# Kernel tuning notes

Measured on AMD Instinct MI355X. Metric: run time of the kernel, lower is better.

Reference implementation:

```python
import jax, jax.numpy as jnp
import numpy as np

# MACE TensorProductConv with in_irreps=128x0e, sh_irreps=0e+1o+2e+3o,
# every CG path 0e (x) l -> l is the identity, so the fused tensor product is
# out[e, c, (l, m)] = w[e, l, c] * x_src[e, c] * sh[e, (l, m)].
# SymmetricContraction is a stub (pass) in the given source, treated as identity.

N_SRC = 10000
N_DST = 10000
E = 100000
C = 128           # channel multiplicity
LS = (0, 1, 2, 3) # spherical-harmonic degrees; dims 1,3,5,7 -> sh dim 16
SH_DIM = sum(2 * l + 1 for l in LS)
MLP_IN = 64
MLP_HID = 128
W_NUMEL = len(LS) * C  # 512 tensor-product weights per edge


def setup_inputs() -> dict:
    key = jax.random.key(0)
    ks = jax.random.split(key, 7)
    return {
        "src_features": jax.random.normal(ks[0], (N_SRC, C), dtype=jnp.float32),
        "edge_sh": jax.random.normal(ks[1], (E, SH_DIM), dtype=jnp.float32),
        "edge_emb": jax.random.normal(ks[2], (E, MLP_IN), dtype=jnp.float32),
        "W1": jax.random.normal(ks[3], (MLP_IN, MLP_HID), dtype=jnp.float32),
        "W2": jax.random.normal(ks[4], (MLP_HID, W_NUMEL), dtype=jnp.float32),
        "src": jax.random.randint(ks[5], (E,), 0, N_SRC),
        "dst": jax.random.randint(ks[6], (E,), 0, N_DST),
        "num_dst_nodes": N_DST,
    }


def _mlp(edge_emb, W1, W2):
    # e3nn FullyConnectedNet: normalized linear layers, silu on hidden only.
    h = jax.nn.silu(edge_emb @ (W1 / np.sqrt(MLP_IN)))
    return h @ (W2 / np.sqrt(MLP_HID))  # [E, W_NUMEL]


def reference(src_features, edge_sh, edge_emb, W1, W2, src, dst, num_dst_nodes):
    tp_w = _mlp(edge_emb, W1, W2).reshape(-1, len(LS), C)  # [E, L, C]
    x_src = src_features[src]                                # gather: [E, C]
    outs = []
    off = 0
    for i, l in enumerate(LS):
        d = 2 * l + 1
        sh_l = edge_sh[:, off:off + d]                       # [E, d]
        # weighted scalar-times-SH tensor product: [E, C, d]
        o = (tp_w[:, i, :] * x_src)[:, :, None] * sh_l[:, None, :]
        outs.append(o.reshape(o.shape[0], C * d))
        off += d
    out_e = jnp.concatenate(outs, axis=-1)                   # [E, 2048]
    # scatter-reduce sum onto destination nodes
    node_out = jax.ops.segment_sum(out_e, dst, num_segments=num_dst_nodes)
    # SymmetricContraction stub -> identity
    return node_out
```

## Files before the change

### kernel.cpp

```cpp
#include <hip/hip_runtime.h>
#include <math.h>

#define C_DIM 128
#define SHD   16
#define HID   128
#define MIN_D 64
#define OUT_PER_NODE 2048
#define BLK   256
#define MBLK  512
#define SCAN_T 1024
#define MT    128

#define HST 136

typedef __attribute__((ext_vector_type(8))) short bf16x8;
typedef __attribute__((ext_vector_type(4))) float f32x4;

__device__ __forceinline__ unsigned f2bf_u(float x) {
    unsigned u = __builtin_bit_cast(unsigned, x);
    return (u + 0x7fffu + ((u >> 16) & 1u)) >> 16;
}
__device__ __forceinline__ short f2bf(float x) { return (short)f2bf_u(x); }
__device__ __forceinline__ unsigned packbf2(float a, float b) {
    return f2bf_u(a) | (f2bf_u(b) << 16);
}
__device__ __forceinline__ float bf2f(unsigned h) {
    return __builtin_bit_cast(float, h << 16);
}

__global__ void prep_kernel(const int* __restrict__ dst, int* counts, int E,
                            const float* __restrict__ W1, const float* __restrict__ W2,
                            short* __restrict__ w1t, short* __restrict__ w2t,
                            int HB) {
    int b = blockIdx.x;
    int t = threadIdx.x;
    if (b < HB) {
        int i = b * BLK + t;
        if (i < E) atomicAdd(&counts[dst[i]], 1);
    } else {
        int i = (b - HB) * BLK + t;
        if (i < MIN_D * HID) {
            int n = i >> 6, k = i & 63;
            w1t[i] = f2bf(W1[k * HID + n] * 0.125f);
        } else if (i < MIN_D * HID + HID * 512) {
            int j = i - MIN_D * HID;
            int p = j >> 7, ks = j & 127;
            int nt = p >> 4, m16 = p & 15;
            int jcol = 32 * (nt >> 1) + 2 * m16 + (nt & 1);
            int ka   = (2 * (ks >> 5) + (ks & 1)) * 16 + ((ks >> 1) & 15);
            w2t[j] = f2bf(W2[ka * 512 + jcol] * 0.0883883476483184f);
        }
    }
}

__global__ __launch_bounds__(SCAN_T)
void scan_kernel(const int* __restrict__ counts, int* row_ptr, int* cursor, int n) {
    const int t = threadIdx.x;
    const int per = (n + SCAN_T - 1) / SCAN_T;
    int lp[16];
    int base = t * per;
    int sum = 0;
    for (int i = 0; i < per && i < 16; ++i) {
        int idx = base + i;
        int v = (idx < n) ? counts[idx] : 0;
        lp[i] = sum;
        sum += v;
    }
    __shared__ int sbuf[SCAN_T];
    sbuf[t] = sum;
    __syncthreads();
    for (int off = 1; off < SCAN_T; off <<= 1) {
        int v = (t >= off) ? sbuf[t - off] : 0;
        __syncthreads();
        sbuf[t] += v;
        __syncthreads();
    }
    int excl = (t == 0) ? 0 : sbuf[t - 1];
    for (int i = 0; i < per && i < 16; ++i) {
        int idx = base + i;
        if (idx < n) {
            int rp = excl + lp[i];
            row_ptr[idx] = rp;
            cursor[idx]  = rp;
        }
    }
    if (t == SCAN_T - 1) row_ptr[n] = sbuf[SCAN_T - 1];
}

__global__ void scatter_kernel(const int* __restrict__ dst, const int* __restrict__ src,
                               int* cursor, int2* es_list, int E) {
    int i = blockIdx.x * blockDim.x + threadIdx.x;
    if (i < E) {
        int pos = atomicAdd(&cursor[dst[i]], 1);
        es_list[pos] = make_int2(i, src[i]);
    }
}

__global__ __launch_bounds__(MBLK)
void mlp_kernel(const float* __restrict__ edge_emb,
                const short* __restrict__ w1t,
                const short* __restrict__ w2t,
                unsigned* __restrict__ tp_u,
                int E)
{
    const int t    = threadIdx.x;
    const int lane = t & 63;
    const int w    = t >> 6;
    const int m16  = lane & 15;
    const int q    = lane >> 4;
    const int e0   = blockIdx.x * MT;

    __shared__ __align__(16) short hb[MT * HST];
    unsigned* hb_u = (unsigned*)hb;

    union CVT { unsigned u[4]; bf16x8 v; };

    bf16x8 a[2];
    {
        const int row = e0 + w * 16 + m16;
        if (row < E) {
            const float* rp = &edge_emb[(size_t)row * MIN_D];
#pragma unroll
            for (int ks = 0; ks < 2; ++ks) {
                float4 v0 = *(const float4*)&rp[ks * 32 + q * 8];
                float4 v1 = *(const float4*)&rp[ks * 32 + q * 8 + 4];
                CVT c;
                c.u[0] = packbf2(v0.x, v0.y);
                c.u[1] = packbf2(v0.z, v0.w);
                c.u[2] = packbf2(v1.x, v1.y);
                c.u[3] = packbf2(v1.z, v1.w);
                a[ks] = c.v;
            }
        } else {
            CVT c; c.u[0] = c.u[1] = c.u[2] = c.u[3] = 0u;
            a[0] = c.v; a[1] = c.v;
        }
    }

#pragma unroll
    for (int u2 = 0; u2 < 4; ++u2) {
        f32x4 c0 = {0.f, 0.f, 0.f, 0.f}, c1 = {0.f, 0.f, 0.f, 0.f};
#pragma unroll
        for (int ks = 0; ks < 2; ++ks) {
            bf16x8 b0 = *(const bf16x8*)&w1t[((2 * u2) * 16 + m16) * MIN_D + ks * 32 + q * 8];
            bf16x8 b1 = *(const bf16x8*)&w1t[((2 * u2 + 1) * 16 + m16) * MIN_D + ks * 32 + q * 8];
            c0 = __builtin_amdgcn_mfma_f32_16x16x32_bf16(a[ks], b0, c0, 0, 0, 0);
            c1 = __builtin_amdgcn_mfma_f32_16x16x32_bf16(a[ks], b1, c1, 0, 0, 0);
        }
#pragma unroll
        for (int r = 0; r < 4; ++r) {
            int hrow = w * 16 + q * 4 + r;
            float z0 = c0[r], z1 = c1[r];
            float h0 = z0 / (1.f + __expf(-z0));
            float h1 = z1 / (1.f + __expf(-z1));
            hb_u[hrow * (HST / 2) + 16 * u2 + m16] = packbf2(h0, h1);
        }
    }

    bf16x8 B[4][4];
#pragma unroll
    for (int j = 0; j < 4; ++j)
#pragma unroll
        for (int ks = 0; ks < 4; ++ks)
            B[j][ks] = *(const bf16x8*)&w2t[((4 * w + j) * 16 + m16) * HID + ks * 32 + q * 8];

    __syncthreads();

    for (int mt = 0; mt < 8; ++mt) {
        bf16x8 av[4];
#pragma unroll
        for (int ks = 0; ks < 4; ++ks)
            av[ks] = *(const bf16x8*)&hb[(mt * 16 + m16) * HST + ks * 32 + q * 8];
        f32x4 acc[4];
#pragma unroll
        for (int j = 0; j < 4; ++j) acc[j] = (f32x4){0.f, 0.f, 0.f, 0.f};
#pragma unroll
        for (int ks = 0; ks < 4; ++ks)
#pragma unroll
            for (int j = 0; j < 4; ++j)
                acc[j] = __builtin_amdgcn_mfma_f32_16x16x32_bf16(av[ks], B[j][ks], acc[j], 0, 0, 0);
#pragma unroll
        for (int i = 0; i < 2; ++i) {
            const int p = 2 * w + i;
#pragma unroll
            for (int r = 0; r < 4; ++r) {
                int e = e0 + mt * 16 + q * 4 + r;
                if (e < E)
                    tp_u[(size_t)e * 256 + 16 * p + m16] = packbf2(acc[2 * i][r], acc[2 * i + 1][r]);
            }
        }
    }
}

template<int L>
__device__ __forceinline__ void tp_node(
    const float* __restrict__ src_features,
    const float* __restrict__ edge_sh,
    const unsigned* __restrict__ tp_u,
    const int2* __restrict__ es_list,
    float* __restrict__ out,
    int n, int t, int rbeg, int rend)
{
    constexpr int D = 2 * L + 1;
    constexpr int SHOFF = L * L;
    const int c0 = (2 * t) & 127;
    const int obase = 128 * L * L + c0 * D;

    float accA[D], accB[D];
#pragma unroll
    for (int m = 0; m < D; ++m) { accA[m] = 0.f; accB[m] = 0.f; }

    int i = rbeg;
    for (; i + 4 <= rend; i += 4) {
        int2 es[4];
#pragma unroll
        for (int k = 0; k < 4; ++k) es[k] = es_list[i + k];
        unsigned tp2[4]; float2 x[4]; float sh[4][D];
#pragma unroll
        for (int k = 0; k < 4; ++k) {
            tp2[k] = tp_u[(size_t)es[k].x * 256 + t];
            x[k]   = *(const float2*)&src_features[(size_t)es[k].y * C_DIM + c0];
            const float* shp = &edge_sh[(size_t)es[k].x * SHD + SHOFF];
#pragma unroll
            for (int m = 0; m < D; ++m) sh[k][m] = shp[m];
        }
#pragma unroll
        for (int k = 0; k < 4; ++k) {
            float wx0 = bf2f(tp2[k] & 0xffffu) * x[k].x;
            float wx1 = bf2f(tp2[k] >> 16)     * x[k].y;
#pragma unroll
            for (int m = 0; m < D; ++m) {
                accA[m] += wx0 * sh[k][m];
                accB[m] += wx1 * sh[k][m];
            }
        }
    }
    for (; i < rend; ++i) {
        int2 es = es_list[i];
        unsigned tp2 = tp_u[(size_t)es.x * 256 + t];
        float2 x = *(const float2*)&src_features[(size_t)es.y * C_DIM + c0];
        float wx0 = bf2f(tp2 & 0xffffu) * x.x;
        float wx1 = bf2f(tp2 >> 16)     * x.y;
        const float* shp = &edge_sh[(size_t)es.x * SHD + SHOFF];
#pragma unroll
        for (int m = 0; m < D; ++m) {
            float sh = shp[m];
            accA[m] += wx0 * sh;
            accB[m] += wx1 * sh;
        }
    }

    float* op = out + (size_t)n * OUT_PER_NODE + obase;
#pragma unroll
    for (int m = 0; m < D; ++m) op[m] = accA[m];
#pragma unroll
    for (int m = 0; m < D; ++m) op[D + m] = accB[m];
}

__global__ __launch_bounds__(BLK)
void tp_kernel(const float* __restrict__ src_features,
               const float* __restrict__ edge_sh,
               const unsigned* __restrict__ tp_u,
               const int* __restrict__ row_ptr,
               const int2* __restrict__ es_list,
               float* __restrict__ out)
{
    const int n = blockIdx.x;
    const int t = threadIdx.x;
    const int l = t >> 6;
    const int rbeg = row_ptr[n];
    const int rend = row_ptr[n + 1];
    if (l == 0)      tp_node<0>(src_features, edge_sh, tp_u, es_list, out, n, t, rbeg, rend);
    else if (l == 1) tp_node<1>(src_features, edge_sh, tp_u, es_list, out, n, t, rbeg, rend);
    else if (l == 2) tp_node<2>(src_features, edge_sh, tp_u, es_list, out, n, t, rbeg, rend);
    else             tp_node<3>(src_features, edge_sh, tp_u, es_list, out, n, t, rbeg, rend);
}


extern "C" void kernel_launch(void* const* d_in, const int* in_sizes, int n_in,
                              void* d_out, int out_size, void* d_ws, size_t ws_size,
                              hipStream_t stream) {
    const float* src_features = (const float*)d_in[0];
    const float* edge_sh      = (const float*)d_in[1];
    const float* edge_emb     = (const float*)d_in[2];
    const float* W1           = (const float*)d_in[3];
    const float* W2           = (const float*)d_in[4];
    const int*   src          = (const int*)d_in[5];
    const int*   dst          = (const int*)d_in[6];

    const int E     = in_sizes[5];
    const int N_DST = out_size / OUT_PER_NODE;
    const int EB    = (E + MT - 1) / MT;

    char* p = (char*)d_ws;
    short* w1t      = (short*)p;              p += MIN_D * HID * 2;
    short* w2t      = (short*)p;              p += HID * 512 * 2;
    unsigned* tp_u  = (unsigned*)p;           p += (size_t)EB * MT * 1024;
    int2* es_list   = (int2*)p;               p += (size_t)E * 8;
    int* counts     = (int*)p;                p += 16384 * 4;
    int* row_ptr    = (int*)p;                p += 16384 * 4;
    int* cursor     = (int*)p;                p += 16384 * 4;

    const int HB = (E + BLK - 1) / BLK;
    const int CB = (MIN_D * HID + HID * 512 + BLK - 1) / BLK;

    (void)hipMemsetAsync(counts, 0, (size_t)N_DST * 4, stream);
    prep_kernel<<<HB + CB, BLK, 0, stream>>>(dst, counts, E, W1, W2, w1t, w2t, HB);
    scan_kernel<<<1, SCAN_T, 0, stream>>>(counts, row_ptr, cursor, N_DST);
    scatter_kernel<<<(E + 255) / 256, 256, 0, stream>>>(dst, src, cursor, es_list, E);
    mlp_kernel<<<EB, MBLK, 0, stream>>>(edge_emb, w1t, w2t, tp_u, E);
    tp_kernel<<<N_DST, BLK, 0, stream>>>(src_features, edge_sh, tp_u,
                                         row_ptr, es_list, (float*)d_out);
}
```

Baseline: 231.7 us.

## Fuse edge MLP with tensor-product scatter over dst-sorted edge blocks

Merges the MLP and the tensor-product/aggregation kernels into one kernel. Each block handles 64 consecutive dst-sorted edges, computes their MLP weights into LDS, and reduces them per destination segment, so the per-edge bf16 weight buffer no longer makes a round trip through global memory. A new seg_zero kernel builds per-block segment lists and zero-fills nodes whose edges span several blocks. Those split nodes are accumulated with float atomics, which adds atomic traffic and makes summation order non-deterministic. LDS use per block rises to roughly 80KB, which may limit occupancy.

```diff
diff --git a/kernel.cpp b/kernel.cpp
--- a/kernel.cpp
+++ b/kernel.cpp
@@ -7,11 +7,8 @@
 #define MIN_D 64
 #define OUT_PER_NODE 2048
 #define BLK   256
-#define MBLK  512
 #define SCAN_T 1024
-#define MT    128
-
-#define HST 136
+#define EBLK  64
 
 typedef __attribute__((ext_vector_type(8))) short bf16x8;
 typedef __attribute__((ext_vector_type(4))) float f32x4;
@@ -46,7 +43,7 @@
             int j = i - MIN_D * HID;
             int p = j >> 7, ks = j & 127;
             int nt = p >> 4, m16 = p & 15;
-            int jcol = 32 * (nt >> 1) + 2 * m16 + (nt & 1);
+            int jcol = 64 * (nt >> 2) + 4 * m16 + (nt & 3);
             int ka   = (2 * (ks >> 5) + (ks & 1)) * 16 + ((ks >> 1) & 15);
             w2t[j] = f2bf(W2[ka * 512 + jcol] * 0.0883883476483184f);
         }
@@ -96,30 +93,142 @@
     }
 }
 
-__global__ __launch_bounds__(MBLK)
-void mlp_kernel(const float* __restrict__ edge_emb,
-                const short* __restrict__ w1t,
-                const short* __restrict__ w2t,
-                unsigned* __restrict__ tp_u,
-                int E)
+__global__ __launch_bounds__(BLK)
+void seg_zero_kernel(const int* __restrict__ row_ptr, unsigned* __restrict__ seg,
+                     int* __restrict__ segcnt, float* __restrict__ out, int n_dst) {
+    const int n = blockIdx.x;
+    const int t = threadIdx.x;
+    const int rb = row_ptr[n], re = row_ptr[n + 1];
+    if (rb == re) {
+        float4 z = make_float4(0.f, 0.f, 0.f, 0.f);
+        float4* op = (float4*)(out + (size_t)n * OUT_PER_NODE);
+        for (int i = t; i < OUT_PER_NODE / 4; i += BLK) op[i] = z;
+        return;
+    }
+    const int b0 = rb >> 6, b1 = (re - 1) >> 6;
+    const bool full = (b0 == b1);
+    if (t == 0) {
+        for (int b = b0; b <= b1; ++b) {
+            int s = rb - b * EBLK; if (s < 0) s = 0;
+            int e = re - b * EBLK; if (e > EBLK) e = EBLK;
+            int idx = atomicAdd(&segcnt[b], 1);
+            if (idx < EBLK)
+                seg[(size_t)b * EBLK + idx] =
+                    (unsigned)n | ((unsigned)s << 16) | ((unsigned)e << 22)
+                                | (full ? (1u << 31) : 0u);
+        }
+    }
+    if (!full) {
+        float4 z = make_float4(0.f, 0.f, 0.f, 0.f);
+        float4* op = (float4*)(out + (size_t)n * OUT_PER_NODE);
+        for (int i = t; i < OUT_PER_NODE / 4; i += BLK) op[i] = z;
+    }
+}
+
+template<int L>
+__device__ __forceinline__ void tp_seg(
+    const float* __restrict__ src_features,
+    const float* __restrict__ edge_sh,
+    const unsigned* tp_lds,
+    const int2* __restrict__ es_list,
+    float* __restrict__ out,
+    int n, int tq, int p0, int s, int e, bool full)
+{
+    constexpr int D = 2 * L + 1;
+    constexpr int SHOFF = L * L;
+    const int c0 = (2 * tq) & 127;
+
+    float accA[D], accB[D];
+#pragma unroll
+    for (int m = 0; m < D; ++m) { accA[m] = 0.f; accB[m] = 0.f; }
+
+    int i = s;
+    for (; i + 4 <= e; i += 4) {
+        int2 es[4];
+#pragma unroll
+        for (int k = 0; k < 4; ++k) es[k] = es_list[p0 + i + k];
+        unsigned tp2[4]; float2 x[4]; float sh[4][D];
+#pragma unroll
+        for (int k = 0; k < 4; ++k) {
+            tp2[k] = tp_lds[(i + k) * 256 + tq];
+            x[k]   = *(const float2*)&src_features[(size_t)es[k].y * C_DIM + c0];
+            const float* shp = &edge_sh[(size_t)es[k].x * SHD + SHOFF];
+#pragma unroll
+            for (int m = 0; m < D; ++m) sh[k][m] = shp[m];
+        }
+#pragma unroll
+        for (int k = 0; k < 4; ++k) {
+            float wx0 = bf2f(tp2[k] & 0xffffu) * x[k].x;
+            float wx1 = bf2f(tp2[k] >> 16)     * x[k].y;
+#pragma unroll
+            for (int m = 0; m < D; ++m) {
+                accA[m] += wx0 * sh[k][m];
+                accB[m] += wx1 * sh[k][m];
+            }
+        }
+    }
+    for (; i < e; ++i) {
+        int2 es = es_list[p0 + i];
+        unsigned tp2 = tp_lds[i * 256 + tq];
+        float2 x = *(const float2*)&src_features[(size_t)es.y * C_DIM + c0];
+        const float* shp = &edge_sh[(size_t)es.x * SHD + SHOFF];
+        float wx0 = bf2f(tp2 & 0xffffu) * x.x;
+        float wx1 = bf2f(tp2 >> 16)     * x.y;
+#pragma unroll
+        for (int m = 0; m < D; ++m) {
+            float shv = shp[m];
+            accA[m] += wx0 * shv;
+            accB[m] += wx1 * shv;
+        }
+    }
+
+    float* op = out + (size_t)n * OUT_PER_NODE + 128 * SHOFF + c0 * D;
+    if (full) {
+#pragma unroll
+        for (int m = 0; m < D; ++m) op[m] = accA[m];
+#pragma unroll
+        for (int m = 0; m < D; ++m) op[D + m] = accB[m];
+    } else {
+#pragma unroll
+        for (int m = 0; m < D; ++m) atomicAdd(&op[m], accA[m]);
+#pragma unroll
+        for (int m = 0; m < D; ++m) atomicAdd(&op[D + m], accB[m]);
+    }
+}
+
+__global__ __launch_bounds__(512, 4)
+void fused_kernel(const float* __restrict__ edge_emb,
+                  const short* __restrict__ w1t,
+                  const short* __restrict__ w2t,
+                  const float* __restrict__ src_features,
+                  const float* __restrict__ edge_sh,
+                  const int2* __restrict__ es_list,
+                  const unsigned* __restrict__ seg,
+                  const int* __restrict__ segcnt,
+                  float* __restrict__ out,
+                  int E)
 {
     const int t    = threadIdx.x;
     const int lane = t & 63;
     const int w    = t >> 6;
     const int m16  = lane & 15;
     const int q    = lane >> 4;
-    const int e0   = blockIdx.x * MT;
-
-    __shared__ __align__(16) short hb[MT * HST];
-    unsigned* hb_u = (unsigned*)hb;
+    const int b    = blockIdx.x;
+    const int p0   = b * EBLK;
+
+    __shared__ __align__(16) unsigned tp_lds[EBLK * 256];
+    __shared__ __align__(16) unsigned hb[EBLK * 64];
 
     union CVT { unsigned u[4]; bf16x8 v; };
 
-    bf16x8 a[2];
     {
-        const int row = e0 + w * 16 + m16;
-        if (row < E) {
-            const float* rp = &edge_emb[(size_t)row * MIN_D];
+        const int mt = w & 3;
+        const int uh = w >> 2;
+        const int prow = p0 + mt * 16 + m16;
+        bf16x8 a[2];
+        if (prow < E) {
+            const int eid = es_list[prow].x;
+            const float* rp = &edge_emb[(size_t)eid * MIN_D];
 #pragma unroll
             for (int ks = 0; ks < 2; ++ks) {
                 float4 v0 = *(const float4*)&rp[ks * 32 + q * 8];
@@ -135,25 +244,25 @@
             CVT c; c.u[0] = c.u[1] = c.u[2] = c.u[3] = 0u;
             a[0] = c.v; a[1] = c.v;
         }
-    }
-
-#pragma unroll
-    for (int u2 = 0; u2 < 4; ++u2) {
-        f32x4 c0 = {0.f, 0.f, 0.f, 0.f}, c1 = {0.f, 0.f, 0.f, 0.f};
-#pragma unroll
-        for (int ks = 0; ks < 2; ++ks) {
-            bf16x8 b0 = *(const bf16x8*)&w1t[((2 * u2) * 16 + m16) * MIN_D + ks * 32 + q * 8];
-            bf16x8 b1 = *(const bf16x8*)&w1t[((2 * u2 + 1) * 16 + m16) * MIN_D + ks * 32 + q * 8];
-            c0 = __builtin_amdgcn_mfma_f32_16x16x32_bf16(a[ks], b0, c0, 0, 0, 0);
-            c1 = __builtin_amdgcn_mfma_f32_16x16x32_bf16(a[ks], b1, c1, 0, 0, 0);
-        }
-#pragma unroll
-        for (int r = 0; r < 4; ++r) {
-            int hrow = w * 16 + q * 4 + r;
-            float z0 = c0[r], z1 = c1[r];
-            float h0 = z0 / (1.f + __expf(-z0));
-            float h1 = z1 / (1.f + __expf(-z1));
-            hb_u[hrow * (HST / 2) + 16 * u2 + m16] = packbf2(h0, h1);
+#pragma unroll
+        for (int ui = 0; ui < 2; ++ui) {
+            const int u2 = 2 * uh + ui;
+            f32x4 c0 = {0.f, 0.f, 0.f, 0.f}, c1 = {0.f, 0.f, 0.f, 0.f};
+#pragma unroll
+            for (int ks = 0; ks < 2; ++ks) {
+                bf16x8 b0 = *(const bf16x8*)&w1t[((2 * u2)     * 16 + m16) * MIN_D + ks * 32 + q * 8];
+                bf16x8 b1 = *(const bf16x8*)&w1t[((2 * u2 + 1) * 16 + m16) * MIN_D + ks * 32 + q * 8];
+                c0 = __builtin_amdgcn_mfma_f32_16x16x32_bf16(a[ks], b0, c0, 0, 0, 0);
+                c1 = __builtin_amdgcn_mfma_f32_16x16x32_bf16(a[ks], b1, c1, 0, 0, 0);
+            }
+#pragma unroll
+            for (int r = 0; r < 4; ++r) {
+                const int row = mt * 16 + q * 4 + r;
+                float z0 = c0[r], z1 = c1[r];
+                float h0 = z0 / (1.f + __expf(-z0));
+                float h1 = z1 / (1.f + __expf(-z1));
+                hb[(row * 64 + 16 * u2 + m16) ^ ((row & 7) << 2)] = packbf2(h0, h1);
+            }
         }
     }
 
@@ -166,116 +275,54 @@
 
     __syncthreads();
 
-    for (int mt = 0; mt < 8; ++mt) {
-        bf16x8 av[4];
-#pragma unroll
-        for (int ks = 0; ks < 4; ++ks)
-            av[ks] = *(const bf16x8*)&hb[(mt * 16 + m16) * HST + ks * 32 + q * 8];
-        f32x4 acc[4];
-#pragma unroll
-        for (int j = 0; j < 4; ++j) acc[j] = (f32x4){0.f, 0.f, 0.f, 0.f};
-#pragma unroll
-        for (int ks = 0; ks < 4; ++ks)
-#pragma unroll
-            for (int j = 0; j < 4; ++j)
-                acc[j] = __builtin_amdgcn_mfma_f32_16x16x32_bf16(av[ks], B[j][ks], acc[j], 0, 0, 0);
-#pragma unroll
-        for (int i = 0; i < 2; ++i) {
-            const int p = 2 * w + i;
+    {
+        const int d0 = 64 * (w >> 1) + 32 * (w & 1) + 2 * m16;
+#pragma unroll
+        for (int mt = 0; mt < 4; ++mt) {
+            const int row = mt * 16 + m16;
+            bf16x8 av[4];
+#pragma unroll
+            for (int ks = 0; ks < 4; ++ks)
+                av[ks] = *(const bf16x8*)&hb[(row * 64 + ks * 16 + q * 4) ^ ((row & 7) << 2)];
+            f32x4 acc[4];
+#pragma unroll
+            for (int j = 0; j < 4; ++j) acc[j] = (f32x4){0.f, 0.f, 0.f, 0.f};
+#pragma unroll
+            for (int ks = 0; ks < 4; ++ks)
+#pragma unroll
+                for (int j = 0; j < 4; ++j)
+                    acc[j] = __builtin_amdgcn_mfma_f32_16x16x32_bf16(av[ks], B[j][ks], acc[j], 0, 0, 0);
 #pragma unroll
             for (int r = 0; r < 4; ++r) {
-                int e = e0 + mt * 16 + q * 4 + r;
-                if (e < E)
-                    tp_u[(size_t)e * 256 + 16 * p + m16] = packbf2(acc[2 * i][r], acc[2 * i + 1][r]);
-            }
-        }
-    }
-}
-
-template<int L>
-__device__ __forceinline__ void tp_node(
-    const float* __restrict__ src_features,
-    const float* __restrict__ edge_sh,
-    const unsigned* __restrict__ tp_u,
-    const int2* __restrict__ es_list,
-    float* __restrict__ out,
-    int n, int t, int rbeg, int rend)
-{
-    constexpr int D = 2 * L + 1;
-    constexpr int SHOFF = L * L;
-    const int c0 = (2 * t) & 127;
-    const int obase = 128 * L * L + c0 * D;
-
-    float accA[D], accB[D];
-#pragma unroll
-    for (int m = 0; m < D; ++m) { accA[m] = 0.f; accB[m] = 0.f; }
-
-    int i = rbeg;
-    for (; i + 4 <= rend; i += 4) {
-        int2 es[4];
-#pragma unroll
-        for (int k = 0; k < 4; ++k) es[k] = es_list[i + k];
-        unsigned tp2[4]; float2 x[4]; float sh[4][D];
-#pragma unroll
-        for (int k = 0; k < 4; ++k) {
-            tp2[k] = tp_u[(size_t)es[k].x * 256 + t];
-            x[k]   = *(const float2*)&src_features[(size_t)es[k].y * C_DIM + c0];
-            const float* shp = &edge_sh[(size_t)es[k].x * SHD + SHOFF];
-#pragma unroll
-            for (int m = 0; m < D; ++m) sh[k][m] = shp[m];
-        }
-#pragma unroll
-        for (int k = 0; k < 4; ++k) {
-            float wx0 = bf2f(tp2[k] & 0xffffu) * x[k].x;
-            float wx1 = bf2f(tp2[k] >> 16)     * x[k].y;
-#pragma unroll
-            for (int m = 0; m < D; ++m) {
-                accA[m] += wx0 * sh[k][m];
-                accB[m] += wx1 * sh[k][m];
-            }
-        }
-    }
-    for (; i < rend; ++i) {
-        int2 es = es_list[i];
-        unsigned tp2 = tp_u[(size_t)es.x * 256 + t];
-        float2 x = *(const float2*)&src_features[(size_t)es.y * C_DIM + c0];
-        float wx0 = bf2f(tp2 & 0xffffu) * x.x;
-        float wx1 = bf2f(tp2 >> 16)     * x.y;
-        const float* shp = &edge_sh[(size_t)es.x * SHD + SHOFF];
-#pragma unroll
-        for (int m = 0; m < D; ++m) {
-            float sh = shp[m];
-            accA[m] += wx0 * sh;
-            accB[m] += wx1 * sh;
-        }
-    }
-
-    float* op = out + (size_t)n * OUT_PER_NODE + obase;
-#pragma unroll
-    for (int m = 0; m < D; ++m) op[m] = accA[m];
-#pragma unroll
-    for (int m = 0; m < D; ++m) op[D + m] = accB[m];
-}
-
-__global__ __launch_bounds__(BLK)
-void tp_kernel(const float* __restrict__ src_features,
-               const float* __restrict__ edge_sh,
-               const unsigned* __restrict__ tp_u,
-               const int* __restrict__ row_ptr,
-               const int2* __restrict__ es_list,
-               float* __restrict__ out)
-{
-    const int n = blockIdx.x;
-    const int t = threadIdx.x;
-    const int l = t >> 6;
-    const int rbeg = row_ptr[n];
-    const int rend = row_ptr[n + 1];
-    if (l == 0)      tp_node<0>(src_features, edge_sh, tp_u, es_list, out, n, t, rbeg, rend);
-    else if (l == 1) tp_node<1>(src_features, edge_sh, tp_u, es_list, out, n, t, rbeg, rend);
-    else if (l == 2) tp_node<2>(src_features, edge_sh, tp_u, es_list, out, n, t, rbeg, rend);
-    else             tp_node<3>(src_features, edge_sh, tp_u, es_list, out, n, t, rbeg, rend);
-}
-
+                const int el = mt * 16 + q * 4 + r;
+                uint2 u;
+                u.x = packbf2(acc[0][r], acc[1][r]);
+                u.y = packbf2(acc[2][r], acc[3][r]);
+                *(uint2*)&tp_lds[el * 256 + d0] = u;
+            }
+        }
+    }
+
+    __syncthreads();
+
+    {
+        const int half = w >> 2;
+        const int tq   = t & 255;
+        const int l    = tq >> 6;
+        const int nseg = segcnt[b];
+        for (int k = half; k < nseg; k += 2) {
+            const unsigned sw = seg[(size_t)b * EBLK + k];
+            const int  n    = (int)(sw & 0xffffu);
+            const int  s    = (int)((sw >> 16) & 63u);
+            const int  e    = (int)((sw >> 22) & 127u);
+            const bool full = (sw >> 31) != 0u;
+            if (l == 0)      tp_seg<0>(src_features, edge_sh, tp_lds, es_list, out, n, tq, p0, s, e, full);
+            else if (l == 1) tp_seg<1>(src_features, edge_sh, tp_lds, es_list, out, n, tq, p0, s, e, full);
+            else if (l == 2) tp_seg<2>(src_features, edge_sh, tp_lds, es_list, out, n, tq, p0, s, e, full);
+            else             tp_seg<3>(src_features, edge_sh, tp_lds, es_list, out, n, tq, p0, s, e, full);
+        }
+    }
+}
 
 extern "C" void kernel_launch(void* const* d_in, const int* in_sizes, int n_in,
                               void* d_out, int out_size, void* d_ws, size_t ws_size,
@@ -290,25 +337,27 @@
 
     const int E     = in_sizes[5];
     const int N_DST = out_size / OUT_PER_NODE;
-    const int EB    = (E + MT - 1) / MT;
+    const int NB    = (E + EBLK - 1) / EBLK;
 
     char* p = (char*)d_ws;
-    short* w1t      = (short*)p;              p += MIN_D * HID * 2;
-    short* w2t      = (short*)p;              p += HID * 512 * 2;
-    unsigned* tp_u  = (unsigned*)p;           p += (size_t)EB * MT * 1024;
-    int2* es_list   = (int2*)p;               p += (size_t)E * 8;
-    int* counts     = (int*)p;                p += 16384 * 4;
-    int* row_ptr    = (int*)p;                p += 16384 * 4;
-    int* cursor     = (int*)p;                p += 16384 * 4;
+    short* w1t     = (short*)p;    p += MIN_D * HID * 2;
+    short* w2t     = (short*)p;    p += HID * 512 * 2;
+    int2* es_list  = (int2*)p;     p += (size_t)E * 8;
+    unsigned* seg  = (unsigned*)p; p += (size_t)NB * EBLK * 4;
+    int* counts    = (int*)p;      p += 16384 * 4;
+    int* row_ptr   = (int*)p;      p += 16384 * 4;
+    int* cursor    = (int*)p;      p += 16384 * 4;
+    int* segcnt    = (int*)p;      p += (size_t)NB * 4;
 
     const int HB = (E + BLK - 1) / BLK;
     const int CB = (MIN_D * HID + HID * 512 + BLK - 1) / BLK;
 
     (void)hipMemsetAsync(counts, 0, (size_t)N_DST * 4, stream);
+    (void)hipMemsetAsync(segcnt, 0, (size_t)NB * 4, stream);
     prep_kernel<<<HB + CB, BLK, 0, stream>>>(dst, counts, E, W1, W2, w1t, w2t, HB);
     scan_kernel<<<1, SCAN_T, 0, stream>>>(counts, row_ptr, cursor, N_DST);
     scatter_kernel<<<(E + 255) / 256, 256, 0, stream>>>(dst, src, cursor, es_list, E);
-    mlp_kernel<<<EB, MBLK, 0, stream>>>(edge_emb, w1t, w2t, tp_u, E);
-    tp_kernel<<<N_DST, BLK, 0, stream>>>(src_features, edge_sh, tp_u,
-                                         row_ptr, es_list, (float*)d_out);
-}
+    seg_zero_kernel<<<N_DST, BLK, 0, stream>>>(row_ptr, seg, segcnt, (float*)d_out, N_DST);
+    fused_kernel<<<NB, 512, 0, stream>>>(edge_emb, w1t, w2t, src_features, edge_sh,
+                                         es_list, seg, segcnt, (float*)d_out, E);
+}
```

Result: slower. 384.2 us (+65.8%).

## Fuse edge MLP into destination-grouped tensor-product kernel via LDS chunks

Applied to the files above, without the earlier changes.

Removes the separate MLP kernel and its per-edge bf16 weight buffer in global memory. The MLP now runs inside the convolution kernel on 16-edge chunks taken in CSR order, and the per-edge weights stay in LDS. Each block handles 4 destination nodes and walks their edges together, flushing accumulators at node boundaries. This avoids a large global write and re-read of tp weights, at the cost of redundant W2 register loads per chunk, extra barriers, and smaller MFMA batches.

```diff
diff --git a/kernel.cpp b/kernel.cpp
--- a/kernel.cpp
+++ b/kernel.cpp
@@ -7,11 +7,8 @@
 #define MIN_D 64
 #define OUT_PER_NODE 2048
 #define BLK   256
-#define MBLK  512
 #define SCAN_T 1024
-#define MT    128
-
-#define HST 136
+#define G     4
 
 typedef __attribute__((ext_vector_type(8))) short bf16x8;
 typedef __attribute__((ext_vector_type(4))) float f32x4;
@@ -46,7 +43,7 @@
             int j = i - MIN_D * HID;
             int p = j >> 7, ks = j & 127;
             int nt = p >> 4, m16 = p & 15;
-            int jcol = 32 * (nt >> 1) + 2 * m16 + (nt & 1);
+            int jcol = 128 * (nt >> 3) + 8 * m16 + (nt & 7);
             int ka   = (2 * (ks >> 5) + (ks & 1)) * 16 + ((ks >> 1) & 15);
             w2t[j] = f2bf(W2[ka * 512 + jcol] * 0.0883883476483184f);
         }
@@ -96,186 +93,218 @@
     }
 }
 
-__global__ __launch_bounds__(MBLK)
-void mlp_kernel(const float* __restrict__ edge_emb,
-                const short* __restrict__ w1t,
-                const short* __restrict__ w2t,
-                unsigned* __restrict__ tp_u,
-                int E)
+template<int L>
+__device__ __forceinline__ void tp_chunk(
+    const float* __restrict__ src_features,
+    const float* __restrict__ edge_sh,
+    const unsigned* tp_lds,
+    const int2* __restrict__ es_list,
+    const int* __restrict__ row_ptr,
+    float* __restrict__ out,
+    float* accA, float* accB, int& g, int& nextb,
+    int p0, int cnt, int n0, int n_valid, int tq)
+{
+    constexpr int D = 2 * L + 1;
+    constexpr int SHOFF = L * L;
+    const int c0 = (2 * tq) & 127;
+    int i = p0;
+    const int pend = p0 + cnt;
+    while (i < pend && g < n_valid) {
+        const int e = (nextb < pend) ? nextb : pend;
+        int il = i - p0;
+        while (i + 4 <= e) {
+            int2 es[4];
+#pragma unroll
+            for (int k = 0; k < 4; ++k) es[k] = es_list[i + k];
+            unsigned tp2[4]; float2 x[4]; float sh[4][D];
+#pragma unroll
+            for (int k = 0; k < 4; ++k) {
+                tp2[k] = tp_lds[(il + k) * 256 + tq];
+                x[k]   = *(const float2*)&src_features[(size_t)es[k].y * C_DIM + c0];
+                const float* shp = &edge_sh[(size_t)es[k].x * SHD + SHOFF];
+#pragma unroll
+                for (int m = 0; m < D; ++m) sh[k][m] = shp[m];
+            }
+#pragma unroll
+            for (int k = 0; k < 4; ++k) {
+                float wx0 = bf2f(tp2[k] & 0xffffu) * x[k].x;
+                float wx1 = bf2f(tp2[k] >> 16)     * x[k].y;
+#pragma unroll
+                for (int m = 0; m < D; ++m) {
+                    accA[m] += wx0 * sh[k][m];
+                    accB[m] += wx1 * sh[k][m];
+                }
+            }
+            i += 4; il += 4;
+        }
+        while (i < e) {
+            int2 es = es_list[i];
+            unsigned tp2 = tp_lds[il * 256 + tq];
+            float2 x = *(const float2*)&src_features[(size_t)es.y * C_DIM + c0];
+            const float* shp = &edge_sh[(size_t)es.x * SHD + SHOFF];
+            float wx0 = bf2f(tp2 & 0xffffu) * x.x;
+            float wx1 = bf2f(tp2 >> 16)     * x.y;
+#pragma unroll
+            for (int m = 0; m < D; ++m) {
+                float shv = shp[m];
+                accA[m] += wx0 * shv;
+                accB[m] += wx1 * shv;
+            }
+            ++i; ++il;
+        }
+        if (i == nextb) {
+            float* op = out + (size_t)(n0 + g) * OUT_PER_NODE + 128 * SHOFF + c0 * D;
+#pragma unroll
+            for (int m = 0; m < D; ++m) op[m] = accA[m];
+#pragma unroll
+            for (int m = 0; m < D; ++m) op[D + m] = accB[m];
+#pragma unroll
+            for (int m = 0; m < D; ++m) { accA[m] = 0.f; accB[m] = 0.f; }
+            ++g;
+            nextb = (g < n_valid) ? row_ptr[n0 + g + 1] : 0x7fffffff;
+        }
+    }
+}
+
+template<int L>
+__device__ __forceinline__ void tp_flush(
+    float* __restrict__ out, float* accA, float* accB,
+    int& g, int n_valid, int n0, int tq)
+{
+    constexpr int D = 2 * L + 1;
+    constexpr int SHOFF = L * L;
+    const int c0 = (2 * tq) & 127;
+    while (g < n_valid) {
+        float* op = out + (size_t)(n0 + g) * OUT_PER_NODE + 128 * SHOFF + c0 * D;
+#pragma unroll
+        for (int m = 0; m < D; ++m) op[m] = accA[m];
+#pragma unroll
+        for (int m = 0; m < D; ++m) op[D + m] = accB[m];
+#pragma unroll
+        for (int m = 0; m < D; ++m) { accA[m] = 0.f; accB[m] = 0.f; }
+        ++g;
+    }
+}
+
+__global__ __launch_bounds__(BLK, 4)
+void conv_kernel(const float* __restrict__ edge_emb,
+                 const short* __restrict__ w1t,
+                 const short* __restrict__ w2t,
+                 const float* __restrict__ src_features,
+                 const float* __restrict__ edge_sh,
+                 const int* __restrict__ row_ptr,
+                 const int2* __restrict__ es_list,
+                 float* __restrict__ out,
+                 int n_dst)
 {
     const int t    = threadIdx.x;
     const int lane = t & 63;
-    const int w    = t >> 6;
+    const int wv   = t >> 6;
     const int m16  = lane & 15;
     const int q    = lane >> 4;
-    const int e0   = blockIdx.x * MT;
-
-    __shared__ __align__(16) short hb[MT * HST];
-    unsigned* hb_u = (unsigned*)hb;
+
+    const int n0      = blockIdx.x * G;
+    const int n_valid = (n_dst - n0 < G) ? (n_dst - n0) : G;
+    const int rbeg    = row_ptr[n0];
+    const int rend    = row_ptr[n0 + n_valid];
+    const int nch     = (rend - rbeg + 15) >> 4;
+
+    __shared__ __align__(16) unsigned tp_lds[16 * 256];
+    __shared__ __align__(16) unsigned hb[1024];
 
     union CVT { unsigned u[4]; bf16x8 v; };
 
-    bf16x8 a[2];
-    {
-        const int row = e0 + w * 16 + m16;
-        if (row < E) {
-            const float* rp = &edge_emb[(size_t)row * MIN_D];
+    bf16x8 b1a[2], b1b[2];
+#pragma unroll
+    for (int ks = 0; ks < 2; ++ks) {
+        b1a[ks] = *(const bf16x8*)&w1t[((2 * wv)     * 16 + m16) * MIN_D + ks * 32 + q * 8];
+        b1b[ks] = *(const bf16x8*)&w1t[((2 * wv + 1) * 16 + m16) * MIN_D + ks * 32 + q * 8];
+    }
+
+    float accA[7], accB[7];
+#pragma unroll
+    for (int m = 0; m < 7; ++m) { accA[m] = 0.f; accB[m] = 0.f; }
+    int g     = 0;
+    int nextb = row_ptr[n0 + 1];
+
+    for (int c = 0; c < nch; ++c) {
+        const int p0  = rbeg + (c << 4);
+        const int cnt = (rend - p0 < 16) ? (rend - p0) : 16;
+
+        bf16x8 a[2];
+        if (m16 < cnt) {
+            const int eid = es_list[p0 + m16].x;
+            const float* rp = &edge_emb[(size_t)eid * MIN_D];
 #pragma unroll
             for (int ks = 0; ks < 2; ++ks) {
                 float4 v0 = *(const float4*)&rp[ks * 32 + q * 8];
                 float4 v1 = *(const float4*)&rp[ks * 32 + q * 8 + 4];
-                CVT c;
-                c.u[0] = packbf2(v0.x, v0.y);
-                c.u[1] = packbf2(v0.z, v0.w);
-                c.u[2] = packbf2(v1.x, v1.y);
-                c.u[3] = packbf2(v1.z, v1.w);
-                a[ks] = c.v;
+                CVT cc;
+                cc.u[0] = packbf2(v0.x, v0.y);
+                cc.u[1] = packbf2(v0.z, v0.w);
+                cc.u[2] = packbf2(v1.x, v1.y);
+                cc.u[3] = packbf2(v1.z, v1.w);
+                a[ks] = cc.v;
             }
         } else {
-            CVT c; c.u[0] = c.u[1] = c.u[2] = c.u[3] = 0u;
-            a[0] = c.v; a[1] = c.v;
-        }
-    }
-
-#pragma unroll
-    for (int u2 = 0; u2 < 4; ++u2) {
-        f32x4 c0 = {0.f, 0.f, 0.f, 0.f}, c1 = {0.f, 0.f, 0.f, 0.f};
+            CVT cc; cc.u[0] = cc.u[1] = cc.u[2] = cc.u[3] = 0u;
+            a[0] = cc.v; a[1] = cc.v;
+        }
+        f32x4 h0 = {0.f, 0.f, 0.f, 0.f}, h1 = {0.f, 0.f, 0.f, 0.f};
 #pragma unroll
         for (int ks = 0; ks < 2; ++ks) {
-            bf16x8 b0 = *(const bf16x8*)&w1t[((2 * u2) * 16 + m16) * MIN_D + ks * 32 + q * 8];
-            bf16x8 b1 = *(const bf16x8*)&w1t[((2 * u2 + 1) * 16 + m16) * MIN_D + ks * 32 + q * 8];
-            c0 = __builtin_amdgcn_mfma_f32_16x16x32_bf16(a[ks], b0, c0, 0, 0, 0);
-            c1 = __builtin_amdgcn_mfma_f32_16x16x32_bf16(a[ks], b1, c1, 0, 0, 0);
+            h0 = __builtin_amdgcn_mfma_f32_16x16x32_bf16(a[ks], b1a[ks], h0, 0, 0, 0);
+            h1 = __builtin_amdgcn_mfma_f32_16x16x32_bf16(a[ks], b1b[ks], h1, 0, 0, 0);
         }
 #pragma unroll
         for (int r = 0; r < 4; ++r) {
-            int hrow = w * 16 + q * 4 + r;
-            float z0 = c0[r], z1 = c1[r];
-            float h0 = z0 / (1.f + __expf(-z0));
-            float h1 = z1 / (1.f + __expf(-z1));
-            hb_u[hrow * (HST / 2) + 16 * u2 + m16] = packbf2(h0, h1);
-        }
-    }
-
-    bf16x8 B[4][4];
-#pragma unroll
-    for (int j = 0; j < 4; ++j)
-#pragma unroll
-        for (int ks = 0; ks < 4; ++ks)
-            B[j][ks] = *(const bf16x8*)&w2t[((4 * w + j) * 16 + m16) * HID + ks * 32 + q * 8];
-
-    __syncthreads();
-
-    for (int mt = 0; mt < 8; ++mt) {
-        bf16x8 av[4];
-#pragma unroll
-        for (int ks = 0; ks < 4; ++ks)
-            av[ks] = *(const bf16x8*)&hb[(mt * 16 + m16) * HST + ks * 32 + q * 8];
-        f32x4 acc[4];
-#pragma unroll
-        for (int j = 0; j < 4; ++j) acc[j] = (f32x4){0.f, 0.f, 0.f, 0.f};
-#pragma unroll
-        for (int ks = 0; ks < 4; ++ks)
-#pragma unroll
-            for (int j = 0; j < 4; ++j)
-                acc[j] = __builtin_amdgcn_mfma_f32_16x16x32_bf16(av[ks], B[j][ks], acc[j], 0, 0, 0);
-#pragma unroll
-        for (int i = 0; i < 2; ++i) {
-            const int p = 2 * w + i;
+            const int row = q * 4 + r;
+            float z0 = h0[r], z1 = h1[r];
+            float s0 = z0 / (1.f + __expf(-z0));
+            float s1 = z1 / (1.f + __expf(-z1));
+            hb[(row * 64 + 16 * wv + m16) ^ ((row & 7) << 2)] = packbf2(s0, s1);
+        }
+        __syncthreads();
+
+        {
+            bf16x8 av[4];
+#pragma unroll
+            for (int ks = 0; ks < 4; ++ks)
+                av[ks] = *(const bf16x8*)&hb[(m16 * 64 + ks * 16 + q * 4) ^ ((m16 & 7) << 2)];
+            f32x4 p[8];
+#pragma unroll
+            for (int j = 0; j < 8; ++j) p[j] = (f32x4){0.f, 0.f, 0.f, 0.f};
+#pragma unroll
+            for (int ks = 0; ks < 4; ++ks)
+#pragma unroll
+                for (int j = 0; j < 8; ++j) {
+                    bf16x8 B = *(const bf16x8*)&w2t[((8 * wv + j) * 16 + m16) * HID + ks * 32 + q * 8];
+                    p[j] = __builtin_amdgcn_mfma_f32_16x16x32_bf16(av[ks], B, p[j], 0, 0, 0);
+                }
 #pragma unroll
             for (int r = 0; r < 4; ++r) {
-                int e = e0 + mt * 16 + q * 4 + r;
-                if (e < E)
-                    tp_u[(size_t)e * 256 + 16 * p + m16] = packbf2(acc[2 * i][r], acc[2 * i + 1][r]);
-            }
-        }
-    }
-}
-
-template<int L>
-__device__ __forceinline__ void tp_node(
-    const float* __restrict__ src_features,
-    const float* __restrict__ edge_sh,
-    const unsigned* __restrict__ tp_u,
-    const int2* __restrict__ es_list,
-    float* __restrict__ out,
-    int n, int t, int rbeg, int rend)
-{
-    constexpr int D = 2 * L + 1;
-    constexpr int SHOFF = L * L;
-    const int c0 = (2 * t) & 127;
-    const int obase = 128 * L * L + c0 * D;
-
-    float accA[D], accB[D];
-#pragma unroll
-    for (int m = 0; m < D; ++m) { accA[m] = 0.f; accB[m] = 0.f; }
-
-    int i = rbeg;
-    for (; i + 4 <= rend; i += 4) {
-        int2 es[4];
-#pragma unroll
-        for (int k = 0; k < 4; ++k) es[k] = es_list[i + k];
-        unsigned tp2[4]; float2 x[4]; float sh[4][D];
-#pragma unroll
-        for (int k = 0; k < 4; ++k) {
-            tp2[k] = tp_u[(size_t)es[k].x * 256 + t];
-            x[k]   = *(const float2*)&src_features[(size_t)es[k].y * C_DIM + c0];
-            const float* shp = &edge_sh[(size_t)es[k].x * SHD + SHOFF];
-#pragma unroll
-            for (int m = 0; m < D; ++m) sh[k][m] = shp[m];
-        }
-#pragma unroll
-        for (int k = 0; k < 4; ++k) {
-            float wx0 = bf2f(tp2[k] & 0xffffu) * x[k].x;
-            float wx1 = bf2f(tp2[k] >> 16)     * x[k].y;
-#pragma unroll
-            for (int m = 0; m < D; ++m) {
-                accA[m] += wx0 * sh[k][m];
-                accB[m] += wx1 * sh[k][m];
-            }
-        }
-    }
-    for (; i < rend; ++i) {
-        int2 es = es_list[i];
-        unsigned tp2 = tp_u[(size_t)es.x * 256 + t];
-        float2 x = *(const float2*)&src_features[(size_t)es.y * C_DIM + c0];
-        float wx0 = bf2f(tp2 & 0xffffu) * x.x;
-        float wx1 = bf2f(tp2 >> 16)     * x.y;
-        const float* shp = &edge_sh[(size_t)es.x * SHD + SHOFF];
-#pragma unroll
-        for (int m = 0; m < D; ++m) {
-            float sh = shp[m];
-            accA[m] += wx0 * sh;
-            accB[m] += wx1 * sh;
-        }
-    }
-
-    float* op = out + (size_t)n * OUT_PER_NODE + obase;
-#pragma unroll
-    for (int m = 0; m < D; ++m) op[m] = accA[m];
-#pragma unroll
-    for (int m = 0; m < D; ++m) op[D + m] = accB[m];
-}
-
-__global__ __launch_bounds__(BLK)
-void tp_kernel(const float* __restrict__ src_features,
-               const float* __restrict__ edge_sh,
-               const unsigned* __restrict__ tp_u,
-               const int* __restrict__ row_ptr,
-               const int2* __restrict__ es_list,
-               float* __restrict__ out)
-{
-    const int n = blockIdx.x;
-    const int t = threadIdx.x;
-    const int l = t >> 6;
-    const int rbeg = row_ptr[n];
-    const int rend = row_ptr[n + 1];
-    if (l == 0)      tp_node<0>(src_features, edge_sh, tp_u, es_list, out, n, t, rbeg, rend);
-    else if (l == 1) tp_node<1>(src_features, edge_sh, tp_u, es_list, out, n, t, rbeg, rend);
-    else if (l == 2) tp_node<2>(src_features, edge_sh, tp_u, es_list, out, n, t, rbeg, rend);
-    else             tp_node<3>(src_features, edge_sh, tp_u, es_list, out, n, t, rbeg, rend);
-}
-
+                uint4 u;
+                u.x = packbf2(p[0][r], p[1][r]);
+                u.y = packbf2(p[2][r], p[3][r]);
+                u.z = packbf2(p[4][r], p[5][r]);
+                u.w = packbf2(p[6][r], p[7][r]);
+                *(uint4*)&tp_lds[(q * 4 + r) * 256 + 64 * wv + 4 * m16] = u;
+            }
+        }
+
+        if (wv == 0)      tp_chunk<0>(src_features, edge_sh, tp_lds, es_list, row_ptr, out, accA, accB, g, nextb, p0, cnt, n0, n_valid, t);
+        else if (wv == 1) tp_chunk<1>(src_features, edge_sh, tp_lds, es_list, row_ptr, out, accA, accB, g, nextb, p0, cnt, n0, n_valid, t);
+        else if (wv == 2) tp_chunk<2>(src_features, edge_sh, tp_lds, es_list, row_ptr, out, accA, accB, g, nextb, p0, cnt, n0, n_valid, t);
+        else              tp_chunk<3>(src_features, edge_sh, tp_lds, es_list, row_ptr, out, accA, accB, g, nextb, p0, cnt, n0, n_valid, t);
+
+        __syncthreads();
+    }
+
+    if (wv == 0)      tp_flush<0>(out, accA, accB, g, n_valid, n0, t);
+    else if (wv == 1) tp_flush<1>(out, accA, accB, g, n_valid, n0, t);
+    else if (wv == 2) tp_flush<2>(out, accA, accB, g, n_valid, n0, t);
+    else              tp_flush<3>(out, accA, accB, g, n_valid, n0, t);
+}
 
 extern "C" void kernel_launch(void* const* d_in, const int* in_sizes, int n_in,
                               void* d_out, int out_size, void* d_ws, size_t ws_size,
@@ -290,16 +319,15 @@
 
     const int E     = in_sizes[5];
     const int N_DST = out_size / OUT_PER_NODE;
-    const int EB    = (E + MT - 1) / MT;
+    const int NBC   = (N_DST + G - 1) / G;
 
     char* p = (char*)d_ws;
-    short* w1t      = (short*)p;              p += MIN_D * HID * 2;
-    short* w2t      = (short*)p;              p += HID * 512 * 2;
-    unsigned* tp_u  = (unsigned*)p;           p += (size_t)EB * MT * 1024;
-    int2* es_list   = (int2*)p;               p += (size_t)E * 8;
-    int* counts     = (int*)p;                p += 16384 * 4;
-    int* row_ptr    = (int*)p;                p += 16384 * 4;
-    int* cursor     = (int*)p;                p += 16384 * 4;
+    short* w1t    = (short*)p;  p += MIN_D * HID * 2;
+    short* w2t    = (short*)p;  p += HID * 512 * 2;
+    int2* es_list = (int2*)p;   p += (size_t)E * 8;
+    int* counts   = (int*)p;    p += 16384 * 4;
+    int* row_ptr  = (int*)p;    p += 16384 * 4;
+    int* cursor   = (int*)p;    p += 16384 * 4;
 
     const int HB = (E + BLK - 1) / BLK;
     const int CB = (MIN_D * HID + HID * 512 + BLK - 1) / BLK;
@@ -308,7 +336,6 @@
     prep_kernel<<<HB + CB, BLK, 0, stream>>>(dst, counts, E, W1, W2, w1t, w2t, HB);
     scan_kernel<<<1, SCAN_T, 0, stream>>>(counts, row_ptr, cursor, N_DST);
     scatter_kernel<<<(E + 255) / 256, 256, 0, stream>>>(dst, src, cursor, es_list, E);
-    mlp_kernel<<<EB, MBLK, 0, stream>>>(edge_emb, w1t, w2t, tp_u, E);
-    tp_kernel<<<N_DST, BLK, 0, stream>>>(src_features, edge_sh, tp_u,
-                                         row_ptr, es_list, (float*)d_out);
-}
+    conv_kernel<<<NBC, BLK, 0, stream>>>(edge_emb, w1t, w2t, src_features, edge_sh,
+                                         row_ptr, es_list, (float*)d_out, N_DST);
+}
```

Result: slower. 450.0 us (+94.2%).
